# Kernel optimization log

Hardware: AMD Instinct MI355X
Metric: run time of the kernel (lower is better)

## Reference

```python
import jax, jax.numpy as jnp
import numpy as np
from jax import lax

B, S, D = 1, 1024, 1024
E, TOP_K = 8, 2
F_TEXT, F_VIS = 512, 256
N_SHARED = 2
F_SHARED = F_TEXT * N_SHARED  # 1024
NORM_MIN = 1e-12


def setup_inputs() -> dict:
    key = jax.random.key(0)
    ks = jax.random.split(key, 16)
    s = 0.02
    return {
        "hidden_states": jax.random.normal(ks[0], (B, S, D), jnp.float32),
        "mm_token_type_ids": jax.random.randint(ks[1], (B, S), 0, 2, jnp.int32),
        # text sparse MoE
        "text_router_w": jax.random.normal(ks[2], (E, D), jnp.float32) * s,
        "text_score_bias": jax.random.normal(ks[3], (E,), jnp.float32) * s,
        "text_wg": jax.random.normal(ks[4], (E, D, F_TEXT), jnp.float32) * s,
        "text_wu": jax.random.normal(ks[5], (E, D, F_TEXT), jnp.float32) * s,
        "text_wd": jax.random.normal(ks[6], (E, F_TEXT, D), jnp.float32) * s,
        # vision sparse MoE
        "vision_router_w": jax.random.normal(ks[7], (E, D), jnp.float32) * s,
        "vision_score_bias": jax.random.normal(ks[8], (E,), jnp.float32) * s,
        "vision_wg": jax.random.normal(ks[9], (E, D, F_VIS), jnp.float32) * s,
        "vision_wu": jax.random.normal(ks[10], (E, D, F_VIS), jnp.float32) * s,
        "vision_wd": jax.random.normal(ks[11], (E, F_VIS, D), jnp.float32) * s,
        # shared experts (single SwiGLU MLP, inter = F_TEXT * N_SHARED)
        "shared_wg": jax.random.normal(ks[12], (D, F_SHARED), jnp.float32) * s,
        "shared_wu": jax.random.normal(ks[13], (D, F_SHARED), jnp.float32) * s,
        "shared_wd": jax.random.normal(ks[14], (F_SHARED, D), jnp.float32) * s,
    }


def _sparse_moe(x, w_router, score_bias, wg, wu, wd):
    """x: [T,D] fp32. Returns (out [T,D], router_logits [T,E])."""
    logits = x @ w_router.T                                   # [T,E] fp32
    probs = jax.nn.softmax(logits, axis=-1)
    # correction bias biases the top-k SELECTION only
    _, idx = lax.top_k(probs + score_bias[None, :], TOP_K)    # [T,K]
    w = jnp.take_along_axis(probs, idx, axis=-1)              # [T,K]
    w = w / jnp.clip(jnp.sum(w, axis=-1, keepdims=True), NORM_MIN)
    T = x.shape[0]
    # dense combine matrix: zeros except routing weights at selected experts
    comb = jnp.zeros((T, E), x.dtype).at[jnp.arange(T)[:, None], idx].add(w)
    def step(acc, expert):
        g, u, d, c = expert                                   # [D,F],[D,F],[F,D],[T]
        h = jax.nn.silu(x @ g) * (x @ u)                      # [T,F]
        return acc + c[:, None] * (h @ d), None
    out, _ = lax.scan(step, jnp.zeros_like(x), (wg, wu, wd, comb.T))
    return out, logits


def reference(hidden_states, mm_token_type_ids,
              text_router_w, text_score_bias, text_wg, text_wu, text_wd,
              vision_router_w, vision_score_bias, vision_wg, vision_wu, vision_wd,
              shared_wg, shared_wu, shared_wd):
    b, s, d = hidden_states.shape
    x = hidden_states.reshape(-1, d)                          # [T,D]
    # shared experts run on every token
    shared = (jax.nn.silu(x @ shared_wg) * (x @ shared_wu)) @ shared_wd
    # modality-isolated MoE: torch gathers text/vision subsets; per-token math
    # is independent, so compute both and select (identical values).
    t_out, t_log = _sparse_moe(x, text_router_w, text_score_bias, text_wg, text_wu, text_wd)
    v_out, v_log = _sparse_moe(x, vision_router_w, vision_score_bias, vision_wg, vision_wu, vision_wd)
    is_vis = (mm_token_type_ids.reshape(-1) != 0)             # [T]
    out = jnp.where(is_vis[:, None], v_out, t_out) + shared
    router_logits = jnp.where(is_vis[:, None], v_log, t_log)  # [T,E]
    return out.reshape(b, s, d), router_logits
```

## Files before the change

### kernel.cpp

```cpp
#include <hip/hip_runtime.h>

typedef short bf16x8 __attribute__((ext_vector_type(8)));
typedef float f32x4 __attribute__((ext_vector_type(4)));
typedef ushort ushort8 __attribute__((ext_vector_type(8)));

#define DIM 1024
#define MAXSLOT 4096
#define PREP_TBLKS 1088

__device__ __forceinline__ ushort f2bf(float f) {
  unsigned u = __float_as_uint(f);
  u += 0x7fffu + ((u >> 16) & 1u);
  return (ushort)(u >> 16);
}

__device__ __forceinline__ void gld16(const ushort* g, ushort* l) {
  __builtin_amdgcn_global_load_lds(
      (const __attribute__((address_space(1))) unsigned int*)g,
      (__attribute__((address_space(3))) unsigned int*)l, 16, 0, 0);
}

__device__ __forceinline__ void transpose_slab(
    const float* __restrict__ src, ushort* __restrict__ dst,
    int K, int C, int kb, int nb0, int nbcnt, uint* tile0, uint* tile1) {
  int k0 = kb << 6;
  int tid = threadIdx.x;
  int tx = tid & 15, ty = tid >> 4;
  int sx = tid & 7,  sy = tid >> 3;
  int kt = K >> 6;
  uint* bufs[2] = {tile0, tile1};
  float4 v[4];

  auto loadT = [&](int nb) {
#pragma unroll
    for (int p = 0; p < 2; ++p)
#pragma unroll
      for (int q = 0; q < 2; ++q)
        v[p * 2 + q] = *(const float4*)(
            src + (size_t)(k0 + (p * 16 + ty) * 2 + q) * C + (nb << 6) + tx * 4);
  };
  auto packW = [&](uint* buf) {
#pragma unroll
    for (int p = 0; p < 2; ++p) {
      uint u[4];
#pragma unroll
      for (int c = 0; c < 4; ++c) {
        float lo = ((const float*)&v[p * 2])[c];
        float hi = ((const float*)&v[p * 2 + 1])[c];
        u[c] = (uint)f2bf(lo) | ((uint)f2bf(hi) << 16);
      }
      *(uint4*)&buf[(p * 16 + ty) * 65 + tx * 4] = *(uint4*)u;
    }
  };

  loadT(nb0); packW(bufs[0]);
  __syncthreads();
  for (int i = 0; i < nbcnt; ++i) {
    bool more = i + 1 < nbcnt;
    if (more) loadT(nb0 + i + 1);
    uint* cur = bufs[i & 1];
    ushort* tb = dst + ((size_t)(nb0 + i) * kt + kb) * 4096;
#pragma unroll
    for (int p = 0; p < 2; ++p) {
      int n = p * 32 + sy;
      ushort8 o;
#pragma unroll
      for (int jj = 0; jj < 4; ++jj) {
        uint u = cur[(4 * sx + jj) * 65 + n];
        o[2 * jj]     = (ushort)(u & 0xffff);
        o[2 * jj + 1] = (ushort)(u >> 16);
      }
      *(ushort8*)(tb + n * 64 + sx * 8) = o;
    }
    if (more) packW(bufs[(i + 1) & 1]);
    __syncthreads();
  }
}


__global__ __launch_bounds__(256) void prep_router_kernel(
    const float* __restrict__ s_wg, const float* __restrict__ s_wu,
    const float* __restrict__ t_wg, const float* __restrict__ t_wu,
    const float* __restrict__ v_wg, const float* __restrict__ v_wu,
    ushort* __restrict__ swgT, ushort* __restrict__ swuT,
    ushort* __restrict__ twgT, ushort* __restrict__ twuT,
    ushort* __restrict__ vwgT, ushort* __restrict__ vwuT,
    const float* __restrict__ x, const int* __restrict__ tt,
    const float* __restrict__ t_rw, const float* __restrict__ t_bias,
    const float* __restrict__ v_rw, const float* __restrict__ v_bias,
    int4* __restrict__ ti, float2* __restrict__ tw,
    float* __restrict__ logits_out, ushort* __restrict__ xb) {
  __shared__ uint tile[2][32 * 65];
  int b = blockIdx.x;
  if (b >= PREP_TBLKS) {
    int t = (b - PREP_TBLKS) * 4 + (threadIdx.x >> 6);
    int lane = threadIdx.x & 63;
    const float* xr = x + (size_t)t * DIM;
    int vis = tt[t] != 0;
    const float* rw   = vis ? v_rw   : t_rw;
    const float* bias = vis ? v_bias : t_bias;
    float4 xv[4];
#pragma unroll
    for (int i = 0; i < 4; ++i) {
      xv[i] = *(const float4*)(xr + lane * 4 + 256 * i);
      ushort4 o;
      o.x = f2bf(xv[i].x); o.y = f2bf(xv[i].y);
      o.z = f2bf(xv[i].z); o.w = f2bf(xv[i].w);
      *(ushort4*)(xb + (size_t)t * DIM + lane * 4 + 256 * i) = o;
    }
    float lg[8];
#pragma unroll
    for (int e = 0; e < 8; ++e) {
      const float* wrow = rw + (size_t)e * DIM;
      float s = 0.f;
#pragma unroll
      for (int i = 0; i < 4; ++i) {
        float4 wv = *(const float4*)(wrow + lane * 4 + 256 * i);
        s += xv[i].x * wv.x + xv[i].y * wv.y + xv[i].z * wv.z + xv[i].w * wv.w;
      }
#pragma unroll
      for (int off = 32; off > 0; off >>= 1) s += __shfl_xor(s, off);
      lg[e] = s;
    }
    if (lane == 0) {
      float mx = lg[0];
      for (int e = 1; e < 8; ++e) mx = fmaxf(mx, lg[e]);
      float ex[8]; float sum = 0.f;
      for (int e = 0; e < 8; ++e) { ex[e] = __expf(lg[e] - mx); sum += ex[e]; }
      float inv = 1.f / sum;
      float pr[8], sc[8];
      for (int e = 0; e < 8; ++e) { pr[e] = ex[e] * inv; sc[e] = pr[e] + bias[e]; }
      int i0 = 0;
      for (int e = 1; e < 8; ++e) if (sc[e] > sc[i0]) i0 = e;
      int i1 = -1;
      for (int e = 0; e < 8; ++e) {
        if (e == i0) continue;
        if (i1 < 0 || sc[e] > sc[i1]) i1 = e;
      }
      float w0 = pr[i0], w1 = pr[i1];
      float s2 = fmaxf(w0 + w1, 1e-12f);
      w0 /= s2; w1 /= s2;
      ti[t] = make_int4(i0 | (vis << 8), 0, i1, 0);
      tw[t] = make_float2(w0, w1);
      for (int e = 0; e < 8; ++e) logits_out[(size_t)t * 8 + e] = lg[e];
    }
    return;
  }
  const float* src; ushort* dst; int K = 1024, C, kb, half;
  if (b < 64) {
    int m = b >> 5; int r = b & 31; kb = r >> 1; half = r & 1;
    src = m ? s_wu : s_wg; dst = m ? swuT : swgT; C = 1024;
  } else if (b < 320) {
    int i = b - 64; int e = i >> 5; int r = i & 31; kb = r >> 1; half = r & 1;
    src = t_wg + (size_t)e * 524288; dst = twgT + (size_t)e * 524288; C = 512;
  } else if (b < 576) {
    int i = b - 320; int e = i >> 5; int r = i & 31; kb = r >> 1; half = r & 1;
    src = t_wu + (size_t)e * 524288; dst = twuT + (size_t)e * 524288; C = 512;
  } else if (b < 832) {
    int i = b - 576; int e = i >> 5; int r = i & 31; kb = r >> 1; half = r & 1;
    src = v_wg + (size_t)e * 262144; dst = vwgT + (size_t)e * 262144; C = 256;
  } else {
    int i = b - 832; int e = i >> 5; int r = i & 31; kb = r >> 1; half = r & 1;
    src = v_wu + (size_t)e * 262144; dst = vwuT + (size_t)e * 262144; C = 256;
  }
  int nbh = C >> 7;
  transpose_slab(src, dst, K, C, kb, half * nbh, nbh, tile[0], tile[1]);
}

__global__ __launch_bounds__(256) void finalize_kernel(
    int* __restrict__ meta, int4* __restrict__ ti,
    int* __restrict__ tok_text, int* __restrict__ tok_vis) {
  __shared__ int cnt[16];
  __shared__ int sb[16];
  if (threadIdx.x < 16) cnt[threadIdx.x] = 0;
  __syncthreads();
  for (int t = threadIdx.x; t < 1024; t += 256) {
    int4 v = ti[t];
    int e0 = v.x & 0xff, vis = v.x >> 8, e1 = v.z;
    v.y = atomicAdd(&cnt[vis * 8 + e0], 1);
    v.w = atomicAdd(&cnt[vis * 8 + e1], 1);
    ti[t] = v;
  }
  __syncthreads();
  if (threadIdx.x == 0) {
    int bt = 0, tc = 0;
    for (int e = 0; e < 8; ++e) {
      sb[e] = bt; meta[16 + e] = bt;
      int nt = (cnt[e] + 127) >> 7;
      for (int i = 0; i < nt; ++i) meta[40 + tc++] = e;
      bt += nt << 7;
    }
    meta[34] = bt >> 7;
    int bv = 0, vc = 0;
    for (int e = 0; e < 8; ++e) {
      sb[8 + e] = bv; meta[25 + e] = bv;
      int nt = (cnt[8 + e] + 127) >> 7;
      for (int i = 0; i < nt; ++i) meta[72 + vc++] = e;
      bv += nt << 7;
    }
    meta[35] = bv >> 7;
  }
  __syncthreads();
  for (int i = threadIdx.x; i < MAXSLOT; i += 256) { tok_text[i] = 0; tok_vis[i] = 0; }
  __syncthreads();
  for (int t = threadIdx.x; t < 1024; t += 256) {
    int4 v = ti[t];
    int e0 = v.x & 0xff, vis = v.x >> 8, e1 = v.z;
    int* tl = vis ? tok_vis : tok_text;
    tl[sb[vis * 8 + e0] + v.y] = t;
    tl[sb[vis * 8 + e1] + v.w] = t;
  }
}

__global__ __launch_bounds__(256) void up_kernel(
    const ushort* __restrict__ Xb,
    const ushort* __restrict__ swgT, const ushort* __restrict__ swuT,
    const ushort* __restrict__ twgT, const ushort* __restrict__ twuT,
    const ushort* __restrict__ vwgT, const ushort* __restrict__ vwuT,
    const float* __restrict__ s_wd, const float* __restrict__ t_wd,
    const float* __restrict__ v_wd,
    ushort* __restrict__ swdT, ushort* __restrict__ twdT,
    ushort* __restrict__ vwdT,
    const int* __restrict__ meta,
    const int* __restrict__ tok_text, const int* __restrict__ tok_vis,
    ushort* __restrict__ H_sh, ushort* __restrict__ H_tx,
    ushort* __restrict__ H_vs) {
  __shared__ ushort smem[2][16384];
  int b = blockIdx.x;
  int tid = threadIdx.x, lane = tid & 63, w = tid >> 6;

  if (b >= 512) {
    int i = b - 512;
    const float* src; ushort* dst; int K, kb, q;
    if (i < 64) {
      kb = i >> 2; q = i & 3; src = s_wd; dst = swdT; K = 1024;
    } else if (i < 320) {
      int j = i - 64; int e = j >> 5; int r = j & 31; kb = r >> 2; q = r & 3;
      src = t_wd + (size_t)e * 524288; dst = twdT + (size_t)e * 524288; K = 512;
    } else {
      int j = i - 320; int e = j >> 4; int r = j & 15; kb = r >> 2; q = r & 3;
      src = v_wd + (size_t)e * 262144; dst = vwdT + (size_t)e * 262144; K = 256;
    }
    uint* t0 = (uint*)&smem[0][0];
    uint* t1 = t0 + 32 * 65;
    transpose_slab(src, dst, K, 1024, kb, q * 4, 4, t0, t1);
    return;
  }

  int wm = w >> 1, wn = w & 1;
  int fr = lane & 15, fq = lane >> 4;
  int l8 = lane >> 3, l7 = lane & 7;
  int sw = (l7 ^ l8) * 8;

  const ushort *Bg, *Bu;
  const int* tl = nullptr;
  ushort* Hout; int hstride, t0, ncol0;
  if (b < 128) {
    int mt = b >> 4, ng = b & 15;
    t0 = mt * 128; ncol0 = ng * 64;
    Bg = swgT + (size_t)ng * 65536; Bu = swuT + (size_t)ng * 65536;
    Hout = H_sh; hstride = 1024;
  } else if (b < 384) {
    int rel = b - 128; int mt = rel >> 3, ng = rel & 7;
    if (mt >= meta[34]) return;
    int e = meta[40 + mt];
    t0 = mt * 128; ncol0 = ng * 64;
    Bg = twgT + (size_t)e * 524288 + (size_t)ng * 65536;
    Bu = twuT + (size_t)e * 524288 + (size_t)ng * 65536;
    tl = tok_text; Hout = H_tx; hstride = 512;
  } else {
    int rel = b - 384; int mt = rel >> 2, ng = rel & 3;
    if (mt >= meta[35]) return;
    int e = meta[72 + mt];
    t0 = mt * 128; ncol0 = ng * 64;
    Bg = vwgT + (size_t)e * 262144 + (size_t)ng * 65536;
    Bu = vwuT + (size_t)e * 262144 + (size_t)ng * 65536;
    tl = tok_vis; Hout = H_vs; hstride = 256;
  }

  const ushort* aptr[4];
#pragma unroll
  for (int i = 0; i < 4; ++i) {
    int row = (w * 4 + i) * 8 + l8;
    int tok = tl ? tl[t0 + row] : (t0 + row);
    aptr[i] = Xb + (size_t)tok * DIM + sw;
  }
  const ushort *bgp[2], *bup[2];
#pragma unroll
  for (int i = 0; i < 2; ++i) {
    int row = (w * 2 + i) * 8 + l8;
    bgp[i] = Bg + row * 64 + sw;
    bup[i] = Bu + row * 64 + sw;
  }

  auto stage = [&](int buf, int k0, int koffB) {
    ushort* base = smem[buf];
#pragma unroll
    for (int i = 0; i < 4; ++i)
      gld16(aptr[i] + k0, base + (w * 4 + i) * 512);
#pragma unroll
    for (int i = 0; i < 2; ++i) {
      gld16(bgp[i] + koffB, base + 8192 + (w * 2 + i) * 512);
      gld16(bup[i] + koffB, base + 12288 + (w * 2 + i) * 512);
    }
  };

  f32x4 accg[4][2] = {}; f32x4 accu[4][2] = {};
  int sl[2] = { ((0 * 4 + fq) ^ (fr & 7)) * 8, ((1 * 4 + fq) ^ (fr & 7)) * 8 };

  stage(0, 0, 0);
  __syncthreads();
  for (int t = 0; t < 16; ++t) {
    int cur = t & 1;
    if (t < 15) stage(cur ^ 1, (t + 1) * 64, (t + 1) * 4096);
    const ushort* pA = smem[cur];
    const ushort* pBg = smem[cur] + 8192;
    const ushort* pBu = smem[cur] + 12288;
#pragma unroll
    for (int kk = 0; kk < 2; ++kk) {
      bf16x8 a[4], bg[2], bu[2];
#pragma unroll
      for (int m = 0; m < 4; ++m)
        a[m] = *(const bf16x8*)&pA[(wm * 64 + m * 16 + fr) * 64 + sl[kk]];
#pragma unroll
      for (int n = 0; n < 2; ++n) {
        bg[n] = *(const bf16x8*)&pBg[(wn * 32 + n * 16 + fr) * 64 + sl[kk]];
        bu[n] = *(const bf16x8*)&pBu[(wn * 32 + n * 16 + fr) * 64 + sl[kk]];
      }
#pragma unroll
      for (int m = 0; m < 4; ++m)
#pragma unroll
        for (int n = 0; n < 2; ++n) {
          accg[m][n] = __builtin_amdgcn_mfma_f32_16x16x32_bf16(a[m], bg[n], accg[m][n], 0, 0, 0);
          accu[m][n] = __builtin_amdgcn_mfma_f32_16x16x32_bf16(a[m], bu[n], accu[m][n], 0, 0, 0);
        }
    }
    __syncthreads();
  }

#pragma unroll
  for (int m = 0; m < 4; ++m) {
    int rb = t0 + wm * 64 + m * 16 + fq * 4;
#pragma unroll
    for (int n = 0; n < 2; ++n) {
      int col = ncol0 + wn * 32 + n * 16 + fr;
#pragma unroll
      for (int r = 0; r < 4; ++r) {
        float g = accg[m][n][r], u = accu[m][n][r];
        float h = g / (1.f + __expf(-g)) * u;
        Hout[(size_t)(rb + r) * hstride + col] = f2bf(h);
      }
    }
  }
}

__global__ __launch_bounds__(256) void down_kernel(
    const ushort* __restrict__ H_sh, const ushort* __restrict__ H_tx,
    const ushort* __restrict__ H_vs,
    const ushort* __restrict__ swdT, const ushort* __restrict__ twdT,
    const ushort* __restrict__ vwdT,
    const int* __restrict__ meta, float* __restrict__ out,
    float* __restrict__ pd_tx, float* __restrict__ pd_vs) {
  __shared__ ushort smem[2][16384];
  int b = blockIdx.x;
  int tid = threadIdx.x, lane = tid & 63, w = tid >> 6;
  int wm = w >> 1, wn = w & 1;
  int fr = lane & 15, fq = lane >> 4;
  int l8 = lane >> 3, l7 = lane & 7;
  int sw = (l7 ^ l8) * 8;

  const ushort *A, *Bt; float* O;
  int ksteps, astride, t0, n0;
  if (b < 64) {
    int mt = b >> 3, nt = b & 7;
    t0 = mt * 128; n0 = nt * 128;
    A = H_sh; astride = 1024; Bt = swdT; ksteps = 16;
    O = out;
  } else if (b < 320) {
    int rel = b - 64; int mt = rel >> 3, nt = rel & 7;
    if (mt >= meta[34]) return;
    int e = meta[40 + mt];
    t0 = mt * 128; n0 = nt * 128;
    A = H_tx; astride = 512;
    Bt = twdT + (size_t)e * 524288; ksteps = 8;
    O = pd_tx;
  } else {
    int rel = b - 320; int mt = rel >> 3, nt = rel & 7;
    if (mt >= meta[35]) return;
    int e = meta[72 + mt];
    t0 = mt * 128; n0 = nt * 128;
    A = H_vs; astride = 256;
    Bt = vwdT + (size_t)e * 262144; ksteps = 4;
    O = pd_vs;
  }

  const ushort *aptr[4], *bptr[4];
#pragma unroll
  for (int i = 0; i < 4; ++i) {
    int c = w * 4 + i;
    int row = c * 8 + l8;
    aptr[i] = A + (size_t)(t0 + row) * astride + sw;
    int nb = (n0 >> 6) + (c >> 3);
    int rowin = row & 63;
    bptr[i] = Bt + (size_t)nb * ksteps * 4096 + rowin * 64 + sw;
  }

  auto stage = [&](int buf, int k0, int koffB) {
    ushort* base = smem[buf];
#pragma unroll
    for (int i = 0; i < 4; ++i) {
      gld16(aptr[i] + k0, base + (w * 4 + i) * 512);
      gld16(bptr[i] + koffB, base + 8192 + (w * 4 + i) * 512);
    }
  };

  f32x4 acc[4][4] = {};
  int sl[2] = { ((0 * 4 + fq) ^ (fr & 7)) * 8, ((1 * 4 + fq) ^ (fr & 7)) * 8 };

  stage(0, 0, 0);
  __syncthreads();
  for (int t = 0; t < ksteps; ++t) {
    int cur = t & 1;
    if (t + 1 < ksteps) stage(cur ^ 1, (t + 1) * 64, (t + 1) * 4096);
    const ushort* pA = smem[cur];
    const ushort* pB = smem[cur] + 8192;
#pragma unroll
    for (int kk = 0; kk < 2; ++kk) {
      bf16x8 a[4], bb[4];
#pragma unroll
      for (int m = 0; m < 4; ++m)
        a[m] = *(const bf16x8*)&pA[(wm * 64 + m * 16 + fr) * 64 + sl[kk]];
#pragma unroll
      for (int n = 0; n < 4; ++n)
        bb[n] = *(const bf16x8*)&pB[(wn * 64 + n * 16 + fr) * 64 + sl[kk]];
#pragma unroll
      for (int m = 0; m < 4; ++m)
#pragma unroll
        for (int n = 0; n < 4; ++n)
          acc[m][n] = __builtin_amdgcn_mfma_f32_16x16x32_bf16(a[m], bb[n], acc[m][n], 0, 0, 0);
    }
    __syncthreads();
  }

#pragma unroll
  for (int m = 0; m < 4; ++m)
#pragma unroll
    for (int n = 0; n < 4; ++n)
#pragma unroll
      for (int r = 0; r < 4; ++r)
        O[(size_t)(t0 + wm * 64 + m * 16 + fq * 4 + r) * DIM
          + n0 + wn * 64 + n * 16 + fr] = acc[m][n][r];
}

__global__ __launch_bounds__(256) void combine_kernel(
    const int4* __restrict__ ti, const float2* __restrict__ tw,
    const int* __restrict__ meta,
    const float* __restrict__ pd_tx, const float* __restrict__ pd_vs,
    float* __restrict__ out) {
  int t = blockIdx.x;
  int4 v = ti[t]; float2 wv = tw[t];
  int e0 = v.x & 0xff, vis = v.x >> 8, e1 = v.z;
  const int* base = meta + (vis ? 25 : 16);
  const float* pd = vis ? pd_vs : pd_tx;
  size_t s0 = base[e0] + v.y, s1 = base[e1] + v.w;
  int d = threadIdx.x * 4;
  f32x4 a  = *(const f32x4*)(out + (size_t)t * DIM + d);
  f32x4 p0 = *(const f32x4*)(pd + s0 * DIM + d);
  f32x4 p1 = *(const f32x4*)(pd + s1 * DIM + d);
#pragma unroll
  for (int j = 0; j < 4; ++j) a[j] = a[j] + wv.x * p0[j] + wv.y * p1[j];
  *(f32x4*)(out + (size_t)t * DIM + d) = a;
}

extern "C" void kernel_launch(void* const* d_in, const int* in_sizes, int n_in,
                              void* d_out, int out_size, void* d_ws, size_t ws_size,
                              hipStream_t stream) {
  const float* x    = (const float*)d_in[0];
  const int*   tt   = (const int*)d_in[1];
  const float* t_rw = (const float*)d_in[2];
  const float* t_b  = (const float*)d_in[3];
  const float* t_wg = (const float*)d_in[4];
  const float* t_wu = (const float*)d_in[5];
  const float* t_wd = (const float*)d_in[6];
  const float* v_rw = (const float*)d_in[7];
  const float* v_b  = (const float*)d_in[8];
  const float* v_wg = (const float*)d_in[9];
  const float* v_wu = (const float*)d_in[10];
  const float* v_wd = (const float*)d_in[11];
  const float* s_wg = (const float*)d_in[12];
  const float* s_wu = (const float*)d_in[13];
  const float* s_wd = (const float*)d_in[14];
  float* out    = (float*)d_out;
  float* logits = out + (size_t)1024 * 1024;

  char* p = (char*)d_ws;
  auto alloc = [&](size_t bytes) {
    char* r = p; p += (bytes + 255) & ~(size_t)255; return r;
  };
  ushort* xb     = (ushort*)alloc((size_t)1024 * 1024 * 2);
  int4*   ti     = (int4*)alloc((size_t)1024 * 16);
  float2* tw     = (float2*)alloc((size_t)1024 * 8);
  int*    meta   = (int*)alloc(512 * 4);
  int*    tok_tx = (int*)alloc(MAXSLOT * 4);
  int*    tok_vs = (int*)alloc(MAXSLOT * 4);
  ushort* swdT   = (ushort*)alloc((size_t)1024 * 1024 * 2);
  ushort* twdT   = (ushort*)alloc((size_t)8 * 1024 * 512 * 2);
  ushort* vwdT   = (ushort*)alloc((size_t)8 * 1024 * 256 * 2);
  ushort* H_sh   = (ushort*)alloc((size_t)1024 * 1024 * 2);
  ushort* H_tx   = (ushort*)alloc((size_t)MAXSLOT * 512 * 2);
  ushort* H_vs   = (ushort*)alloc((size_t)MAXSLOT * 256 * 2);
  char* upmark = p;
  ushort* swgT   = (ushort*)alloc((size_t)1024 * 1024 * 2);
  ushort* swuT   = (ushort*)alloc((size_t)1024 * 1024 * 2);
  ushort* twgT   = (ushort*)alloc((size_t)8 * 512 * 1024 * 2);
  ushort* twuT   = (ushort*)alloc((size_t)8 * 512 * 1024 * 2);
  ushort* vwgT   = (ushort*)alloc((size_t)8 * 256 * 1024 * 2);
  ushort* vwuT   = (ushort*)alloc((size_t)8 * 256 * 1024 * 2);
  float* pd_tx = (float*)upmark;
  float* pd_vs = (float*)(upmark + (size_t)MAXSLOT * DIM * 4);

  prep_router_kernel<<<PREP_TBLKS + 256, 256, 0, stream>>>(
      s_wg, s_wu, t_wg, t_wu, v_wg, v_wu,
      swgT, swuT, twgT, twuT, vwgT, vwuT,
      x, tt, t_rw, t_b, v_rw, v_b, ti, tw, logits, xb);
  finalize_kernel<<<1, 256, 0, stream>>>(meta, ti, tok_tx, tok_vs);
  up_kernel<<<960, 256, 0, stream>>>(xb, swgT, swuT, twgT, twuT, vwgT, vwuT,
                                     s_wd, t_wd, v_wd, swdT, twdT, vwdT,
                                     meta, tok_tx, tok_vs, H_sh, H_tx, H_vs);
  down_kernel<<<576, 256, 0, stream>>>(H_sh, H_tx, H_vs, swdT, twdT, vwdT,
                                       meta, out, pd_tx, pd_vs);
  combine_kernel<<<1024, 256, 0, stream>>>(ti, tw, meta, pd_tx, pd_vs, out);
}
```

Before: 70.68 us.

## Fuse expert combine into down-projection epilogue via weighted atomic scatter-add

Removes the separate combine kernel and the per-slot partial-output buffers. The down-projection kernel now scales each routed row by its routing weight and atomically adds it into the token's output row, and the shared-expert tile also atomically adds. The output is zeroed with a memset up front. This saves a launch and the write and re-read of the fp32 partial buffers, at the cost of many scattered fp32 atomics and a non-deterministic summation order.

New measurement: 80.15 us. 13.4% more time.

```diff
diff --git a/kernel.cpp b/kernel.cpp
--- a/kernel.cpp
+++ b/kernel.cpp
@@ -168,8 +168,9 @@
 }
 
 __global__ __launch_bounds__(256) void finalize_kernel(
-    int* __restrict__ meta, int4* __restrict__ ti,
-    int* __restrict__ tok_text, int* __restrict__ tok_vis) {
+    int* __restrict__ meta, int4* __restrict__ ti, const float2* __restrict__ tw,
+    int* __restrict__ tok_text, int* __restrict__ tok_vis,
+    float* __restrict__ sw_text, float* __restrict__ sw_vis) {
   __shared__ int cnt[16];
   __shared__ int sb[16];
   if (threadIdx.x < 16) cnt[threadIdx.x] = 0;
@@ -201,14 +202,20 @@
     meta[35] = bv >> 7;
   }
   __syncthreads();
-  for (int i = threadIdx.x; i < MAXSLOT; i += 256) { tok_text[i] = 0; tok_vis[i] = 0; }
+  for (int i = threadIdx.x; i < MAXSLOT; i += 256) {
+    tok_text[i] = 0; tok_vis[i] = 0;
+    sw_text[i] = 0.f; sw_vis[i] = 0.f;
+  }
   __syncthreads();
   for (int t = threadIdx.x; t < 1024; t += 256) {
     int4 v = ti[t];
+    float2 wv = tw[t];
     int e0 = v.x & 0xff, vis = v.x >> 8, e1 = v.z;
     int* tl = vis ? tok_vis : tok_text;
-    tl[sb[vis * 8 + e0] + v.y] = t;
-    tl[sb[vis * 8 + e1] + v.w] = t;
+    float* wl = vis ? sw_vis : sw_text;
+    int s0 = sb[vis * 8 + e0] + v.y, s1 = sb[vis * 8 + e1] + v.w;
+    tl[s0] = t; wl[s0] = wv.x;
+    tl[s1] = t; wl[s1] = wv.y;
   }
 }
 
@@ -359,8 +366,10 @@
     const ushort* __restrict__ H_vs,
     const ushort* __restrict__ swdT, const ushort* __restrict__ twdT,
     const ushort* __restrict__ vwdT,
-    const int* __restrict__ meta, float* __restrict__ out,
-    float* __restrict__ pd_tx, float* __restrict__ pd_vs) {
+    const int* __restrict__ meta,
+    const int* __restrict__ tok_text, const int* __restrict__ tok_vis,
+    const float* __restrict__ sw_text, const float* __restrict__ sw_vis,
+    float* __restrict__ out) {
   __shared__ ushort smem[2][16384];
   int b = blockIdx.x;
   int tid = threadIdx.x, lane = tid & 63, w = tid >> 6;
@@ -369,13 +378,13 @@
   int l8 = lane >> 3, l7 = lane & 7;
   int sw = (l7 ^ l8) * 8;
 
-  const ushort *A, *Bt; float* O;
+  const ushort *A, *Bt;
+  const int* tl = nullptr; const float* wl = nullptr;
   int ksteps, astride, t0, n0;
   if (b < 64) {
     int mt = b >> 3, nt = b & 7;
     t0 = mt * 128; n0 = nt * 128;
     A = H_sh; astride = 1024; Bt = swdT; ksteps = 16;
-    O = out;
   } else if (b < 320) {
     int rel = b - 64; int mt = rel >> 3, nt = rel & 7;
     if (mt >= meta[34]) return;
@@ -383,7 +392,7 @@
     t0 = mt * 128; n0 = nt * 128;
     A = H_tx; astride = 512;
     Bt = twdT + (size_t)e * 524288; ksteps = 8;
-    O = pd_tx;
+    tl = tok_text; wl = sw_text;
   } else {
     int rel = b - 320; int mt = rel >> 3, nt = rel & 7;
     if (mt >= meta[35]) return;
@@ -391,7 +400,7 @@
     t0 = mt * 128; n0 = nt * 128;
     A = H_vs; astride = 256;
     Bt = vwdT + (size_t)e * 262144; ksteps = 4;
-    O = pd_vs;
+    tl = tok_vis; wl = sw_vis;
   }
 
   const ushort *aptr[4], *bptr[4];
@@ -442,34 +451,32 @@
     __syncthreads();
   }
 
-#pragma unroll
-  for (int m = 0; m < 4; ++m)
-#pragma unroll
-    for (int n = 0; n < 4; ++n)
-#pragma unroll
-      for (int r = 0; r < 4; ++r)
-        O[(size_t)(t0 + wm * 64 + m * 16 + fq * 4 + r) * DIM
-          + n0 + wn * 64 + n * 16 + fr] = acc[m][n][r];
-}
-
-__global__ __launch_bounds__(256) void combine_kernel(
-    const int4* __restrict__ ti, const float2* __restrict__ tw,
-    const int* __restrict__ meta,
-    const float* __restrict__ pd_tx, const float* __restrict__ pd_vs,
-    float* __restrict__ out) {
-  int t = blockIdx.x;
-  int4 v = ti[t]; float2 wv = tw[t];
-  int e0 = v.x & 0xff, vis = v.x >> 8, e1 = v.z;
-  const int* base = meta + (vis ? 25 : 16);
-  const float* pd = vis ? pd_vs : pd_tx;
-  size_t s0 = base[e0] + v.y, s1 = base[e1] + v.w;
-  int d = threadIdx.x * 4;
-  f32x4 a  = *(const f32x4*)(out + (size_t)t * DIM + d);
-  f32x4 p0 = *(const f32x4*)(pd + s0 * DIM + d);
-  f32x4 p1 = *(const f32x4*)(pd + s1 * DIM + d);
-#pragma unroll
-  for (int j = 0; j < 4; ++j) a[j] = a[j] + wv.x * p0[j] + wv.y * p1[j];
-  *(f32x4*)(out + (size_t)t * DIM + d) = a;
+  if (!tl) {
+#pragma unroll
+    for (int m = 0; m < 4; ++m)
+#pragma unroll
+      for (int r = 0; r < 4; ++r) {
+        int row = t0 + wm * 64 + m * 16 + fq * 4 + r;
+#pragma unroll
+        for (int n = 0; n < 4; ++n)
+          atomicAdd(&out[(size_t)row * DIM + n0 + wn * 64 + n * 16 + fr],
+                    acc[m][n][r]);
+      }
+  } else {
+#pragma unroll
+    for (int m = 0; m < 4; ++m)
+#pragma unroll
+      for (int r = 0; r < 4; ++r) {
+        int slot = t0 + wm * 64 + m * 16 + fq * 4 + r;
+        float wgt = wl[slot];
+        if (wgt == 0.f) continue;
+        int tok = tl[slot];
+#pragma unroll
+        for (int n = 0; n < 4; ++n)
+          atomicAdd(&out[(size_t)tok * DIM + n0 + wn * 64 + n * 16 + fr],
+                    wgt * acc[m][n][r]);
+      }
+  }
 }
 
 extern "C" void kernel_launch(void* const* d_in, const int* in_sizes, int n_in,
@@ -503,31 +510,32 @@
   int*    meta   = (int*)alloc(512 * 4);
   int*    tok_tx = (int*)alloc(MAXSLOT * 4);
   int*    tok_vs = (int*)alloc(MAXSLOT * 4);
+  float*  sw_tx  = (float*)alloc(MAXSLOT * 4);
+  float*  sw_vs  = (float*)alloc(MAXSLOT * 4);
   ushort* swdT   = (ushort*)alloc((size_t)1024 * 1024 * 2);
   ushort* twdT   = (ushort*)alloc((size_t)8 * 1024 * 512 * 2);
   ushort* vwdT   = (ushort*)alloc((size_t)8 * 1024 * 256 * 2);
   ushort* H_sh   = (ushort*)alloc((size_t)1024 * 1024 * 2);
   ushort* H_tx   = (ushort*)alloc((size_t)MAXSLOT * 512 * 2);
   ushort* H_vs   = (ushort*)alloc((size_t)MAXSLOT * 256 * 2);
-  char* upmark = p;
   ushort* swgT   = (ushort*)alloc((size_t)1024 * 1024 * 2);
   ushort* swuT   = (ushort*)alloc((size_t)1024 * 1024 * 2);
   ushort* twgT   = (ushort*)alloc((size_t)8 * 512 * 1024 * 2);
   ushort* twuT   = (ushort*)alloc((size_t)8 * 512 * 1024 * 2);
   ushort* vwgT   = (ushort*)alloc((size_t)8 * 256 * 1024 * 2);
   ushort* vwuT   = (ushort*)alloc((size_t)8 * 256 * 1024 * 2);
-  float* pd_tx = (float*)upmark;
-  float* pd_vs = (float*)(upmark + (size_t)MAXSLOT * DIM * 4);
+
+  hipMemsetAsync(out, 0, (size_t)1024 * 1024 * 4, stream);
 
   prep_router_kernel<<<PREP_TBLKS + 256, 256, 0, stream>>>(
       s_wg, s_wu, t_wg, t_wu, v_wg, v_wu,
       swgT, swuT, twgT, twuT, vwgT, vwuT,
       x, tt, t_rw, t_b, v_rw, v_b, ti, tw, logits, xb);
-  finalize_kernel<<<1, 256, 0, stream>>>(meta, ti, tok_tx, tok_vs);
+  finalize_kernel<<<1, 256, 0, stream>>>(meta, ti, tw, tok_tx, tok_vs,
+                                         sw_tx, sw_vs);
   up_kernel<<<960, 256, 0, stream>>>(xb, swgT, swuT, twgT, twuT, vwgT, vwuT,
                                      s_wd, t_wd, v_wd, swdT, twdT, vwdT,
                                      meta, tok_tx, tok_vs, H_sh, H_tx, H_vs);
   down_kernel<<<576, 256, 0, stream>>>(H_sh, H_tx, H_vs, swdT, twdT, vwdT,
-                                       meta, out, pd_tx, pd_vs);
-  combine_kernel<<<1024, 256, 0, stream>>>(ti, tw, meta, pd_tx, pd_vs, out);
-}
+                                       meta, tok_tx, tok_vs, sw_tx, sw_vs, out);
+}
```
